# Optimization experiments

Hardware: AMD Instinct MI355X
Metric: run time of the kernel (lower is better)

The kernel has to match this reference:

```python
import jax, jax.numpy as jnp
import numpy as np

N, K, D, DOUT = 100000, 16, 128, 128

def setup_inputs() -> dict:
    key = jax.random.key(0)
    k1, k2, k3 = jax.random.split(key, 3)
    self_vecs = jax.random.normal(k1, (N, D), dtype=jnp.float32)
    neigh_vecs = jax.random.normal(k2, (N, K, D), dtype=jnp.float32)
    # glorot([input_dim, output_dim])
    limit = np.sqrt(6.0 / (D + DOUT)).astype(np.float32)
    weights = jax.random.uniform(k3, (D, DOUT), dtype=jnp.float32, minval=-limit, maxval=limit)
    return {"self_vecs": self_vecs, "neigh_vecs": neigh_vecs, "weights": weights}

def reference(self_vecs, neigh_vecs, weights):
    # concat self node as an extra "neighbor": [N, K+1, D]
    neigh_self = jnp.concatenate([neigh_vecs, self_vecs[:, None, :]], axis=1)
    # attention scores: query is the self vector, keys are neighbors+self -> [N, K+1]
    score = jnp.einsum('nd,nkd->nk', self_vecs, neigh_self)
    attn = jax.nn.softmax(score, axis=-1)
    # weighted sum of values -> [N, D]
    context = jnp.einsum('nk,nkd->nd', attn, neigh_self)
    out = context @ weights  # [N, DOUT]
    return jax.nn.relu(out)
```

## Files before the change

### kernel.cpp

```cpp
#include <hip/hip_runtime.h>


constexpr int K    = 16;
constexpr int D    = 128;
constexpr int DOUT = 128;
constexpr int WT_PITCH = 136;
constexpr int CT_PITCH = 132;

typedef short bfrag  __attribute__((ext_vector_type(8)));
typedef float afrag  __attribute__((ext_vector_type(4)));

__device__ __forceinline__ unsigned short f2bf(float f) {
    union { float f; unsigned u; } v; v.f = f;
    const unsigned r = v.u + 0x7FFF + ((v.u >> 16) & 1);
    return (unsigned short)(r >> 16);
}
__device__ __forceinline__ float bf2f(unsigned short b) {
    union { unsigned u; float f; } v; v.u = ((unsigned)b) << 16;
    return v.f;
}

__device__ __forceinline__ float wave_allsum(float x) {
    #pragma unroll
    for (int off = 32; off; off >>= 1)
        x += __shfl_xor(x, off);
    return x;
}

#define LOAD_NODE(vv, sv, nabs) do {                                          \
    const int n_ = (nabs);                                                    \
    const float* nbp_ = neigh_vecs + (size_t)n_ * (K * D) + 2 * lane;         \
    _Pragma("unroll")                                                         \
    for (int k = 0; k < K; ++k) vv[k] = *(const float2*)(nbp_ + (size_t)k * D); \
    sv = *(const float2*)(self_vecs + (size_t)n_ * D + 2 * lane);             \
} while (0)

#define CTX_NODE(vv, sv, row) do {                                            \
    float ss_ = sv.x * sv.x + sv.y * sv.y;                                    \
    float sc_[K];                                                             \
    _Pragma("unroll")                                                         \
    for (int k = 0; k < K; ++k) sc_[k] = sv.x * vv[k].x + sv.y * vv[k].y;     \
    ss_ = wave_allsum(ss_);                                                   \
    _Pragma("unroll")                                                         \
    for (int k = 0; k < K; ++k) sc_[k] = wave_allsum(sc_[k]);                 \
    float m_ = ss_;                                                           \
    _Pragma("unroll")                                                         \
    for (int k = 0; k < K; ++k) m_ = fmaxf(m_, sc_[k]);                       \
    float e_ = __expf(ss_ - m_);                                              \
    float sum_ = e_, cx_ = e_ * sv.x, cy_ = e_ * sv.y;                        \
    _Pragma("unroll")                                                         \
    for (int k = 0; k < K; ++k) {                                             \
        const float ek_ = __expf(sc_[k] - m_);                                \
        sum_ += ek_; cx_ += ek_ * vv[k].x; cy_ += ek_ * vv[k].y;              \
    }                                                                         \
    const float inv_ = 1.f / sum_;                                            \
    *(float2*)&Ct[buf][row][2 * lane] = make_float2(cx_ * inv_, cy_ * inv_);  \
} while (0)

__launch_bounds__(512, 3)
__global__ void gat_fused(const float* __restrict__ self_vecs,
                          const float* __restrict__ neigh_vecs,
                          const float* __restrict__ W,
                          float* __restrict__ out,
                          int n_tiles) {
    __shared__ __align__(16) unsigned short Wt[DOUT][WT_PITCH];
    __shared__ __align__(16) float Ct[2][16][CT_PITCH];

    const int tid = threadIdx.x;

    for (int e = tid; e < D * DOUT; e += blockDim.x) {
        const int k = e >> 7, m = e & 127;
        Wt[m][k] = f2bf(W[e]);
    }
    __syncthreads();

    const int lane = tid & 63;
    const int wid  = tid >> 6;
    const int nl   = lane & 15;
    const int kb   = lane >> 4;
    const int r0   = wid * 2;

    float2 vA[K], vB[K], sA, sB;

    int buf = 0;
    int t = blockIdx.x;
    if (t < n_tiles) {
        LOAD_NODE(vA, sA, t * 16 + r0 + 0);
        LOAD_NODE(vB, sB, t * 16 + r0 + 1);
    }
    for (; t < n_tiles; t += gridDim.x, buf ^= 1) {
        const int node0 = t * 16;

        CTX_NODE(vA, sA, r0 + 0);
        CTX_NODE(vB, sB, r0 + 1);
        const int tn = t + gridDim.x;
        if (tn < n_tiles) {
            LOAD_NODE(vA, sA, tn * 16 + r0 + 0);
            LOAD_NODE(vB, sB, tn * 16 + r0 + 1);
        }

        __syncthreads();

        afrag acc;
        #pragma unroll
        for (int r4 = 0; r4 < 4; ++r4) acc[r4] = 0.f;

        #pragma unroll
        for (int kc = 0; kc < 4; ++kc) {
            const float* cp = &Ct[buf][nl][kc * 32 + kb * 8];
            const float4 c0 = *(const float4*)cp;
            const float4 c1 = *(const float4*)(cp + 4);
            const float cf[8] = {c0.x, c0.y, c0.z, c0.w, c1.x, c1.y, c1.z, c1.w};
            bfrag ch, cl;
            #pragma unroll
            for (int i = 0; i < 8; ++i) {
                const unsigned short hh = f2bf(cf[i]);
                ch[i] = (short)hh;
                cl[i] = (short)f2bf(cf[i] - bf2f(hh));
            }
            const bfrag a = *(const bfrag*)&Wt[wid * 16 + nl][kc * 32 + kb * 8];
            acc = __builtin_amdgcn_mfma_f32_16x16x32_bf16(a, ch, acc, 0, 0, 0);
            acc = __builtin_amdgcn_mfma_f32_16x16x32_bf16(a, cl, acc, 0, 0, 0);
        }
        float* orow = out + (size_t)(node0 + nl) * DOUT + kb * 4;
        *(float4*)(orow + wid * 16) =
            make_float4(fmaxf(acc[0], 0.f), fmaxf(acc[1], 0.f),
                        fmaxf(acc[2], 0.f), fmaxf(acc[3], 0.f));
    }
}

extern "C" void kernel_launch(void* const* d_in, const int* in_sizes, int n_in,
                              void* d_out, int out_size, void* d_ws, size_t ws_size,
                              hipStream_t stream) {
    const float* self_vecs = (const float*)d_in[0];
    const float* neigh     = (const float*)d_in[1];
    const float* W         = (const float*)d_in[2];
    float* out = (float*)d_out;

    const int n_nodes = in_sizes[0] / D;
    const int n_tiles = n_nodes / 16;

    const int tpb = 512;
    const int blocks = 768;
    gat_fused<<<dim3(blocks), dim3(tpb), 0, stream>>>(
        self_vecs, neigh, W, out, n_tiles);
}
```

Before: 206.7 us.

## Split each wave into half-waves per node with float4 loads and 5-step reductions

Each wave now handles its two nodes at once: each 32-lane half loads one node's vectors as float4 rather than the whole wave loading float2 per node in turn. Dot-product reductions drop from 6-step full-wave shuffles to 5-step half-wave shuffles, and half as many reductions are issued per wave. Register footprint stays similar, but launch bounds drop from 3 to 2 blocks per CU and the grid shrinks from 768 to 512 blocks to match. Fewer resident waves may reduce the ability to hide memory latency on this bandwidth-bound load.

```diff
diff --git a/kernel.cpp b/kernel.cpp
--- a/kernel.cpp
+++ b/kernel.cpp
@@ -20,44 +20,14 @@
     return v.f;
 }
 
-__device__ __forceinline__ float wave_allsum(float x) {
+__device__ __forceinline__ float half_allsum(float x) {
     #pragma unroll
-    for (int off = 32; off; off >>= 1)
+    for (int off = 1; off <= 16; off <<= 1)
         x += __shfl_xor(x, off);
     return x;
 }
 
-#define LOAD_NODE(vv, sv, nabs) do {                                          \
-    const int n_ = (nabs);                                                    \
-    const float* nbp_ = neigh_vecs + (size_t)n_ * (K * D) + 2 * lane;         \
-    _Pragma("unroll")                                                         \
-    for (int k = 0; k < K; ++k) vv[k] = *(const float2*)(nbp_ + (size_t)k * D); \
-    sv = *(const float2*)(self_vecs + (size_t)n_ * D + 2 * lane);             \
-} while (0)
-
-#define CTX_NODE(vv, sv, row) do {                                            \
-    float ss_ = sv.x * sv.x + sv.y * sv.y;                                    \
-    float sc_[K];                                                             \
-    _Pragma("unroll")                                                         \
-    for (int k = 0; k < K; ++k) sc_[k] = sv.x * vv[k].x + sv.y * vv[k].y;     \
-    ss_ = wave_allsum(ss_);                                                   \
-    _Pragma("unroll")                                                         \
-    for (int k = 0; k < K; ++k) sc_[k] = wave_allsum(sc_[k]);                 \
-    float m_ = ss_;                                                           \
-    _Pragma("unroll")                                                         \
-    for (int k = 0; k < K; ++k) m_ = fmaxf(m_, sc_[k]);                       \
-    float e_ = __expf(ss_ - m_);                                              \
-    float sum_ = e_, cx_ = e_ * sv.x, cy_ = e_ * sv.y;                        \
-    _Pragma("unroll")                                                         \
-    for (int k = 0; k < K; ++k) {                                             \
-        const float ek_ = __expf(sc_[k] - m_);                                \
-        sum_ += ek_; cx_ += ek_ * vv[k].x; cy_ += ek_ * vv[k].y;              \
-    }                                                                         \
-    const float inv_ = 1.f / sum_;                                            \
-    *(float2*)&Ct[buf][row][2 * lane] = make_float2(cx_ * inv_, cy_ * inv_);  \
-} while (0)
-
-__launch_bounds__(512, 3)
+__launch_bounds__(512, 2)
 __global__ void gat_fused(const float* __restrict__ self_vecs,
                           const float* __restrict__ neigh_vecs,
                           const float* __restrict__ W,
@@ -76,27 +46,61 @@
 
     const int lane = tid & 63;
     const int wid  = tid >> 6;
+    const int half = lane >> 5;
+    const int q    = lane & 31;
     const int nl   = lane & 15;
     const int kb   = lane >> 4;
     const int r0   = wid * 2;
 
-    float2 vA[K], vB[K], sA, sB;
+    float4 v[K], sv;
 
     int buf = 0;
     int t = blockIdx.x;
+
     if (t < n_tiles) {
-        LOAD_NODE(vA, sA, t * 16 + r0 + 0);
-        LOAD_NODE(vB, sB, t * 16 + r0 + 1);
+        const int n0 = t * 16 + r0 + half;
+        const float4* nb = (const float4*)(neigh_vecs + (size_t)n0 * (K * D)) + q;
+        #pragma unroll
+        for (int k = 0; k < K; ++k) v[k] = nb[k * 32];
+        sv = ((const float4*)(self_vecs + (size_t)n0 * D))[q];
     }
+
     for (; t < n_tiles; t += gridDim.x, buf ^= 1) {
         const int node0 = t * 16;
 
-        CTX_NODE(vA, sA, r0 + 0);
-        CTX_NODE(vB, sB, r0 + 1);
+        float ss = sv.x * sv.x + sv.y * sv.y + sv.z * sv.z + sv.w * sv.w;
+        float sc[K];
+        #pragma unroll
+        for (int k = 0; k < K; ++k)
+            sc[k] = sv.x * v[k].x + sv.y * v[k].y + sv.z * v[k].z + sv.w * v[k].w;
+        ss = half_allsum(ss);
+        #pragma unroll
+        for (int k = 0; k < K; ++k) sc[k] = half_allsum(sc[k]);
+
+        float m = ss;
+        #pragma unroll
+        for (int k = 0; k < K; ++k) m = fmaxf(m, sc[k]);
+        float e   = __expf(ss - m);
+        float sum = e;
+        float4 cx = make_float4(e * sv.x, e * sv.y, e * sv.z, e * sv.w);
+        #pragma unroll
+        for (int k = 0; k < K; ++k) {
+            const float ek = __expf(sc[k] - m);
+            sum += ek;
+            cx.x += ek * v[k].x; cx.y += ek * v[k].y;
+            cx.z += ek * v[k].z; cx.w += ek * v[k].w;
+        }
+        const float inv = 1.f / sum;
+        *(float4*)&Ct[buf][r0 + half][4 * q] =
+            make_float4(cx.x * inv, cx.y * inv, cx.z * inv, cx.w * inv);
+
         const int tn = t + gridDim.x;
         if (tn < n_tiles) {
-            LOAD_NODE(vA, sA, tn * 16 + r0 + 0);
-            LOAD_NODE(vB, sB, tn * 16 + r0 + 1);
+            const int n0 = tn * 16 + r0 + half;
+            const float4* nb = (const float4*)(neigh_vecs + (size_t)n0 * (K * D)) + q;
+            #pragma unroll
+            for (int k = 0; k < K; ++k) v[k] = nb[k * 32];
+            sv = ((const float4*)(self_vecs + (size_t)n0 * D))[q];
         }
 
         __syncthreads();
@@ -141,7 +145,7 @@
     const int n_tiles = n_nodes / 16;
 
     const int tpb = 512;
-    const int blocks = 768;
+    const int blocks = 512;
     gat_fused<<<dim3(blocks), dim3(tpb), 0, stream>>>(
         self_vecs, neigh, W, out, n_tiles);
 }
```

Result: faster. 191.6 us (-7.3%).
